# Optimization experiments

Measured on AMD Instinct MI355X. Metric: run time of the kernel, lower is better.

## Reference

```python
import jax, jax.numpy as jnp
import numpy as np

EMB = 1024
NEG_INF = float(-2**32 + 1)
EPS_SCALE = 1e-8   # epsilon added to sqrt(scale) in attention_dot
LN_EPS = 1e-5      # torch.nn.LayerNorm default eps


def _layernorm(x, w, b):
    mu = jnp.mean(x, axis=-1, keepdims=True)
    var = jnp.mean(jnp.square(x - mu), axis=-1, keepdims=True)
    return (x - mu) * jax.lax.rsqrt(var + LN_EPS) * w + b


def setup_inputs() -> dict:
    key = jax.random.key(0)
    ks = jax.random.split(key, 6)
    B, Lq, Lk, E = 8, 2048, 2048, EMB
    queries = jax.random.normal(ks[0], (B, Lq, E), dtype=jnp.float32)
    keys = jax.random.normal(ks[1], (B, Lk, E), dtype=jnp.float32)
    query_masks = jnp.ones((B, Lq), dtype=jnp.float32)
    key_masks = jnp.ones((B, Lk), dtype=jnp.float32)
    # xavier_uniform for Linear(E, E): limit = sqrt(6/(E+E))
    lim = float(np.sqrt(6.0 / (E + E)))
    W1 = jax.random.uniform(ks[2], (E, E), minval=-lim, maxval=lim, dtype=jnp.float32)
    b1 = jnp.zeros((E,), dtype=jnp.float32)
    W2 = jax.random.uniform(ks[3], (E, E), minval=-lim, maxval=lim, dtype=jnp.float32)
    b2 = jnp.zeros((E,), dtype=jnp.float32)
    ln_w = jnp.ones((E,), dtype=jnp.float32)
    ln_b = jnp.zeros((E,), dtype=jnp.float32)
    ln2_w = jnp.ones((E,), dtype=jnp.float32)
    ln2_b = jnp.zeros((E,), dtype=jnp.float32)
    return {"queries": queries, "keys": keys, "query_masks": query_masks,
            "key_masks": key_masks, "ln_w": ln_w, "ln_b": ln_b,
            "ln2_w": ln2_w, "ln2_b": ln2_b, "W1": W1, "b1": b1,
            "W2": W2, "b2": b2}


def reference(queries, keys, query_masks, key_masks, ln_w, ln_b, ln2_w, ln2_b, W1, b1, W2, b2):
    E = queries.shape[-1]
    # scores [B, Lq, Lk]
    sim = jnp.einsum('bik,bjk->bij', queries, keys)
    sim = sim / (jnp.sqrt(jnp.float32(max(1.0, E))) + EPS_SCALE)
    # key mask applied pre-softmax
    sim = jnp.where(key_masks[:, None, :] == 0, jnp.float32(NEG_INF), sim)
    sim = jax.nn.softmax(sim, axis=-1)
    # query mask applied post-softmax
    sim = sim * query_masks[:, :, None]
    attn_out = jnp.einsum('bij,bjk->bik', sim, keys)
    # residual + LayerNorm
    x = _layernorm(attn_out + queries, ln_w, ln_b)
    # FFN: Linear -> ReLU -> Linear, residual, LayerNorm
    h = jax.nn.relu(x @ W1.T + b1)
    y = h @ W2.T + b2
    return _layernorm(y + x, ln2_w, ln2_b)
```

## Files before the change

kernel.cpp:

```cpp
#include <hip/hip_runtime.h>
#include <hip/hip_bf16.h>
#include <stdint.h>

#define NB    8
#define LQ    2048
#define LKK   2048
#define EMBD  1024

typedef __bf16 bf16_t;
typedef __bf16 bf16x8 __attribute__((ext_vector_type(8)));
typedef __bf16 bf16x4 __attribute__((ext_vector_type(4)));
typedef float  f32x4  __attribute__((ext_vector_type(4)));

__device__ __forceinline__ bf16_t f2bf(float x) {
  union { float f; uint32_t u; } v; v.f = x;
  uint32_t r = v.u + 0x7fffu + ((v.u >> 16) & 1u);
  uint16_t h = (uint16_t)(r >> 16);
  return __builtin_bit_cast(bf16_t, h);
}

__device__ __forceinline__ float wred_sum(float v) {
#pragma unroll
  for (int o = 32; o; o >>= 1) v += __shfl_xor(v, o);
  return v;
}
__device__ __forceinline__ float wred_max(float v) {
#pragma unroll
  for (int o = 32; o; o >>= 1) v = fmaxf(v, __shfl_xor(v, o));
  return v;
}

template<int EPI>
__global__ __launch_bounds__(512, 2)
void gemm_nt(const bf16_t* __restrict__ A, const bf16_t* __restrict__ B,
             float* __restrict__ Cf, bf16_t* __restrict__ Cb,
             const float* __restrict__ bias, float scale,
             int M, int N, int K, long sA, long sB, long sC)
{
  __shared__ __align__(16) bf16_t Al[2][8][256][8];
  __shared__ __align__(16) bf16_t Bl[2][8][256][8];

  const int tid  = threadIdx.x;
  const int lane = tid & 63;
  const int wave = tid >> 6;
  const int bz   = blockIdx.z;

  const bf16_t* Ab = A + (long)bz * sA;
  const bf16_t* Bb = B + (long)bz * sB;

  const int bm = blockIdx.x * 256;
  const int bn = blockIdx.y * 256;
  const int wm = (wave >> 2) * 128;
  const int wn = (wave & 3) * 64;

  f32x4 acc[8][4] = {};

  const int srow = tid & 255;
  const int sslc = tid >> 8;

  const int fr = lane & 15;
  const int fs = lane >> 4;

  auto STAGE = [&](int bufi, int kt) {
#pragma unroll
    for (int i = 0; i < 4; i++) {
      const int slc = sslc + 2 * i;
      __builtin_amdgcn_global_load_lds(
        (const __attribute__((address_space(1))) void*)(Ab + (long)(bm + srow) * K + kt + slc * 8),
        (__attribute__((address_space(3))) void*)((char*)&Al[bufi][0][0][0] + (tid + i * 512) * 16),
        16, 0, 0);
    }
#pragma unroll
    for (int i = 0; i < 4; i++) {
      const int slc = sslc + 2 * i;
      __builtin_amdgcn_global_load_lds(
        (const __attribute__((address_space(1))) void*)(Bb + (long)(bn + srow) * K + kt + slc * 8),
        (__attribute__((address_space(3))) void*)((char*)&Bl[bufi][0][0][0] + (tid + i * 512) * 16),
        16, 0, 0);
    }
  };

  auto COMPUTE = [&](int bufi) {
#pragma unroll
    for (int kk = 0; kk < 2; kk++) {
      bf16x8 af[8], bfg[4];
#pragma unroll
      for (int m = 0; m < 8; m++)
        af[m] = *(const bf16x8*)&Al[bufi][4 * kk + fs][wm + m * 16 + fr][0];
#pragma unroll
      for (int n = 0; n < 4; n++)
        bfg[n] = *(const bf16x8*)&Bl[bufi][4 * kk + fs][wn + n * 16 + fr][0];
#pragma unroll
      for (int m = 0; m < 8; m++)
#pragma unroll
        for (int n = 0; n < 4; n++)
          acc[m][n] = __builtin_amdgcn_mfma_f32_16x16x32_bf16(af[m], bfg[n], acc[m][n], 0, 0, 0);
    }
  };

  STAGE(0, 0);
  __syncthreads();
  int buf = 0;
  for (int kt = 64; kt < K; kt += 64) {
    STAGE(buf ^ 1, kt);
    COMPUTE(buf);
    __syncthreads();
    buf ^= 1;
  }
  COMPUTE(buf);

  const int r0 = bm + wm + ((lane >> 4) << 2);
  const int c0 = bn + wn + fr;
  const long cb = (long)bz * sC;
#pragma unroll
  for (int n = 0; n < 4; n++) {
    const int col = c0 + n * 16;
    float bv = 0.0f;
    if constexpr (EPI >= 2) bv = bias[col];
#pragma unroll
    for (int m = 0; m < 8; m++) {
#pragma unroll
      for (int j = 0; j < 4; j++) {
        const int row = r0 + m * 16 + j;
        const long idx = cb + (long)row * N + col;
        float v = acc[m][n][j];
        if constexpr (EPI == 0)      { Cb[idx] = f2bf(v * scale); }
        else if constexpr (EPI == 1) { Cb[idx] = f2bf(v); }
        else if constexpr (EPI == 2) { v += bv; Cb[idx] = f2bf(fmaxf(v, 0.0f)); }
        else                         { v += bv; Cf[idx] = v; }
      }
    }
  }
}

__global__ __launch_bounds__(256)
void softmax_kernel(const bf16_t* __restrict__ S, bf16_t* __restrict__ P,
                    const float* __restrict__ km, const float* __restrict__ qm)
{
  __shared__ float red[8];
  const int r = blockIdx.x;
  const int b = r >> 11;
  const int t = threadIdx.x;
  const bf16_t* row = S + (long)r * LKK;

  const bf16x8 sv = *(const bf16x8*)(row + t * 8);
  const float4 k0 = ((const float4*)(km + (long)b * LKK))[2 * t];
  const float4 k1 = ((const float4*)(km + (long)b * LKK))[2 * t + 1];
  const float kmv[8] = {k0.x, k0.y, k0.z, k0.w, k1.x, k1.y, k1.z, k1.w};

  float v[8];
  float mx = -3.4e38f;
#pragma unroll
  for (int i = 0; i < 8; i++) {
    float s = (float)sv[i];
    s = (kmv[i] == 0.0f) ? -4294967295.0f : s;
    v[i] = s;
    mx = fmaxf(mx, s);
  }
  mx = wred_max(mx);
  if ((t & 63) == 0) red[t >> 6] = mx;
  __syncthreads();
  mx = fmaxf(fmaxf(red[0], red[1]), fmaxf(red[2], red[3]));

  float sum = 0.0f;
#pragma unroll
  for (int i = 0; i < 8; i++) {
    const float e = __expf(v[i] - mx);
    v[i] = e;
    sum += e;
  }
  sum = wred_sum(sum);
  if ((t & 63) == 0) red[4 + (t >> 6)] = sum;
  __syncthreads();
  sum = red[4] + red[5] + red[6] + red[7];

  const float rs = qm[r] / sum;
  bf16x8 o;
#pragma unroll
  for (int i = 0; i < 8; i++) o[i] = f2bf(v[i] * rs);
  *(bf16x8*)(P + (long)r * LKK + t * 8) = o;
}

template<int MODE>
__global__ __launch_bounds__(256)
void ln_kernel(const void* __restrict__ Xv, const void* __restrict__ Rv,
               const float* __restrict__ w, const float* __restrict__ bp,
               void* __restrict__ Yv)
{
  __shared__ float red[8];
  const long r = blockIdx.x;
  const int t = threadIdx.x;

  float x0, x1, x2, x3;
  if constexpr (MODE & 1) {
    const bf16x4 xv = ((const bf16x4*)((const bf16_t*)Xv + r * EMBD))[t];
    x0 = (float)xv[0]; x1 = (float)xv[1]; x2 = (float)xv[2]; x3 = (float)xv[3];
  } else {
    const float4 xv = ((const float4*)((const float*)Xv + r * EMBD))[t];
    x0 = xv.x; x1 = xv.y; x2 = xv.z; x3 = xv.w;
  }
  float r0, r1, r2, r3;
  if constexpr (MODE & 2) {
    const bf16x4 rv = ((const bf16x4*)((const bf16_t*)Rv + r * EMBD))[t];
    r0 = (float)rv[0]; r1 = (float)rv[1]; r2 = (float)rv[2]; r3 = (float)rv[3];
  } else {
    const float4 rv = ((const float4*)((const float*)Rv + r * EMBD))[t];
    r0 = rv.x; r1 = rv.y; r2 = rv.z; r3 = rv.w;
  }
  const float s0 = x0 + r0, s1 = x1 + r1, s2 = x2 + r2, s3 = x3 + r3;

  float sum = wred_sum(s0 + s1 + s2 + s3);
  if ((t & 63) == 0) red[t >> 6] = sum;
  __syncthreads();
  const float mu = (red[0] + red[1] + red[2] + red[3]) * (1.0f / EMBD);

  const float d0 = s0 - mu, d1 = s1 - mu, d2 = s2 - mu, d3 = s3 - mu;
  float sq = wred_sum(d0 * d0 + d1 * d1 + d2 * d2 + d3 * d3);
  if ((t & 63) == 0) red[4 + (t >> 6)] = sq;
  __syncthreads();
  const float var = (red[4] + red[5] + red[6] + red[7]) * (1.0f / EMBD);
  const float rstd = rsqrtf(var + 1e-5f);

  const float4 wv = ((const float4*)w)[t];
  const float4 bv = ((const float4*)bp)[t];
  const float y0 = d0 * rstd * wv.x + bv.x;
  const float y1 = d1 * rstd * wv.y + bv.y;
  const float y2 = d2 * rstd * wv.z + bv.z;
  const float y3 = d3 * rstd * wv.w + bv.w;

  if constexpr (MODE & 4) {
    bf16x4 o; o[0] = f2bf(y0); o[1] = f2bf(y1); o[2] = f2bf(y2); o[3] = f2bf(y3);
    ((bf16x4*)((bf16_t*)Yv + r * EMBD))[t] = o;
  } else {
    ((float4*)((float*)Yv + r * EMBD))[t] = make_float4(y0, y1, y2, y3);
  }
}

__global__ void cvt_kernel(const float* __restrict__ in, bf16_t* __restrict__ out, long n4)
{
  long i = (long)blockIdx.x * 256 + threadIdx.x;
  const long stride = (long)gridDim.x * 256;
  for (; i < n4; i += stride) {
    const float4 v = ((const float4*)in)[i];
    bf16x4 o; o[0] = f2bf(v.x); o[1] = f2bf(v.y); o[2] = f2bf(v.z); o[3] = f2bf(v.w);
    ((bf16x4*)out)[i] = o;
  }
}

__global__ __launch_bounds__(256)
void transpose_cvt(const float* __restrict__ in, bf16_t* __restrict__ out,
                   int rows, int cols)
{
  __shared__ bf16_t tile[32][33];
  const long zb = (long)blockIdx.z * rows * cols;
  const int cb = blockIdx.x * 32;
  const int rb = blockIdx.y * 32;
  const int tx = threadIdx.x & 31;
  const int ty = threadIdx.x >> 5;
#pragma unroll
  for (int i = 0; i < 4; i++) {
    const int rr = ty + i * 8;
    tile[rr][tx] = f2bf(in[zb + (long)(rb + rr) * cols + cb + tx]);
  }
  __syncthreads();
#pragma unroll
  for (int i = 0; i < 4; i++) {
    const int cc = ty + i * 8;
    out[zb + (long)(cb + cc) * rows + rb + tx] = tile[tx][cc];
  }
}

extern "C" void kernel_launch(void* const* d_in, const int* in_sizes, int n_in,
                              void* d_out, int out_size, void* d_ws, size_t ws_size,
                              hipStream_t stream)
{
  const float* q    = (const float*)d_in[0];
  const float* k    = (const float*)d_in[1];
  const float* qm   = (const float*)d_in[2];
  const float* km   = (const float*)d_in[3];
  const float* lnw  = (const float*)d_in[4];
  const float* lnb  = (const float*)d_in[5];
  const float* ln2w = (const float*)d_in[6];
  const float* ln2b = (const float*)d_in[7];
  const float* W1   = (const float*)d_in[8];
  const float* b1   = (const float*)d_in[9];
  const float* W2   = (const float*)d_in[10];
  const float* b2   = (const float*)d_in[11];

  char* ws = (char*)d_ws;
  char* ob = (char*)d_out;
  const float scale = 0.03125f;
  const long MB = 1L << 20;
  const long QE = (long)LQ * EMBD;
  const long SS = (long)LQ * LKK;

  if (ws_size >= 100 * MB) {
    bf16_t* Qb   = (bf16_t*)ws;
    bf16_t* attn = (bf16_t*)ws;
    bf16_t* Kb   = (bf16_t*)(ws + 32 * MB);
    bf16_t* h    = (bf16_t*)(ws + 32 * MB);
    bf16_t* Kt   = (bf16_t*)(ws + 64 * MB);
    bf16_t* W1b  = (bf16_t*)(ws + 96 * MB);
    bf16_t* W2b  = (bf16_t*)(ws + 98 * MB);
    bf16_t* Sb   = (bf16_t*)ob;
    float*  y    = (float*)ob;

    cvt_kernel<<<1024, 256, 0, stream>>>(W1, W1b, (long)EMBD * EMBD / 4);
    cvt_kernel<<<1024, 256, 0, stream>>>(W2, W2b, (long)EMBD * EMBD / 4);
    cvt_kernel<<<4096, 256, 0, stream>>>(q, Qb, (long)NB * QE / 4);
    cvt_kernel<<<4096, 256, 0, stream>>>(k, Kb, (long)NB * QE / 4);
    transpose_cvt<<<dim3(EMBD / 32, LKK / 32, NB), 256, 0, stream>>>(k, Kt, LKK, EMBD);

    gemm_nt<0><<<dim3(LQ / 256, LKK / 256, NB), 512, 0, stream>>>(
        Qb, Kb, nullptr, Sb, nullptr, scale, LQ, LKK, EMBD, QE, QE, SS);
    softmax_kernel<<<NB * LQ, 256, 0, stream>>>(Sb, Sb, km, qm);
    gemm_nt<1><<<dim3(LQ / 256, EMBD / 256, NB), 512, 0, stream>>>(
        Sb, Kt, nullptr, attn, nullptr, 0.0f, LQ, EMBD, LKK, SS, (long)EMBD * LKK, QE);
    ln_kernel<5><<<NB * LQ, 256, 0, stream>>>(attn, q, lnw, lnb, attn);
    gemm_nt<2><<<dim3(NB * LQ / 256, EMBD / 256, 1), 512, 0, stream>>>(
        attn, W1b, nullptr, h, b1, 0.0f, NB * LQ, EMBD, EMBD, 0, 0, 0);
    gemm_nt<3><<<dim3(NB * LQ / 256, EMBD / 256, 1), 512, 0, stream>>>(
        h, W2b, y, nullptr, b2, 0.0f, NB * LQ, EMBD, EMBD, 0, 0, 0);
    ln_kernel<2><<<NB * LQ, 256, 0, stream>>>(y, attn, ln2w, ln2b, y);

  } else if (ws_size >= 52 * MB) {
    bf16_t* attn = (bf16_t*)ws;
    bf16_t* W1b  = (bf16_t*)(ws + 32 * MB);
    bf16_t* W2b  = (bf16_t*)(ws + 34 * MB);
    bf16_t* Kth  = (bf16_t*)(ws + 36 * MB);
    bf16_t* h    = (bf16_t*)(ws + 36 * MB);
    bf16_t* Sb   = (bf16_t*)ob;
    bf16_t* Qbh  = (bf16_t*)(ob + 32 * MB);
    bf16_t* Kbh  = (bf16_t*)(ob + 48 * MB);
    float*  y    = (float*)ob;

    cvt_kernel<<<1024, 256, 0, stream>>>(W1, W1b, (long)EMBD * EMBD / 4);
    cvt_kernel<<<1024, 256, 0, stream>>>(W2, W2b, (long)EMBD * EMBD / 4);

    for (int it = 0; it < 2; it++) {
      const int bo = it * 4;
      const float* qh = q + bo * QE;
      const float* kh = k + bo * QE;
      cvt_kernel<<<2048, 256, 0, stream>>>(qh, Qbh, 4 * QE / 4);
      cvt_kernel<<<2048, 256, 0, stream>>>(kh, Kbh, 4 * QE / 4);
      transpose_cvt<<<dim3(EMBD / 32, LKK / 32, 4), 256, 0, stream>>>(kh, Kth, LKK, EMBD);

      gemm_nt<0><<<dim3(LQ / 256, LKK / 256, 4), 512, 0, stream>>>(
          Qbh, Kbh, nullptr, Sb, nullptr, scale, LQ, LKK, EMBD, QE, QE, SS);
      softmax_kernel<<<4 * LQ, 256, 0, stream>>>(Sb, Sb, km + bo * LKK, qm + bo * LQ);
      gemm_nt<1><<<dim3(LQ / 256, EMBD / 256, 4), 512, 0, stream>>>(
          Sb, Kth, nullptr, attn + bo * QE, nullptr, 0.0f, LQ, EMBD, LKK,
          SS, (long)EMBD * LKK, QE);
    }
    ln_kernel<5><<<NB * LQ, 256, 0, stream>>>(attn, q, lnw, lnb, attn);
    for (int c = 0; c < 2; c++) {
      bf16_t* xc = attn + (long)c * 8192 * EMBD;
      float*  yc = y + (long)c * 8192 * EMBD;
      gemm_nt<2><<<dim3(8192 / 256, EMBD / 256, 1), 512, 0, stream>>>(
          xc, W1b, nullptr, h, b1, 0.0f, 8192, EMBD, EMBD, 0, 0, 0);
      gemm_nt<3><<<dim3(8192 / 256, EMBD / 256, 1), 512, 0, stream>>>(
          h, W2b, yc, nullptr, b2, 0.0f, 8192, EMBD, EMBD, 0, 0, 0);
    }
    ln_kernel<2><<<NB * LQ, 256, 0, stream>>>(y, attn, ln2w, ln2b, y);

  } else {
    if (ws_size < 44 * MB) return;
    bf16_t* attn = (bf16_t*)ws;
    bf16_t* W1b  = (bf16_t*)(ws + 32 * MB);
    bf16_t* W2b  = (bf16_t*)(ws + 34 * MB);
    bf16_t* h    = (bf16_t*)(ws + 36 * MB);
    bf16_t* Sb   = (bf16_t*)(ob);
    bf16_t* Pb   = (bf16_t*)(ob + 8 * MB);
    bf16_t* Qbb  = (bf16_t*)(ob + 16 * MB);
    bf16_t* Kbb  = (bf16_t*)(ob + 20 * MB);
    bf16_t* Ktb  = (bf16_t*)(ob + 24 * MB);

    cvt_kernel<<<1024, 256, 0, stream>>>(W1, W1b, (long)EMBD * EMBD / 4);
    cvt_kernel<<<1024, 256, 0, stream>>>(W2, W2b, (long)EMBD * EMBD / 4);

    for (int b = 0; b < NB; b++) {
      const float* qb = q + b * QE;
      const float* kb = k + b * QE;
      cvt_kernel<<<2048, 256, 0, stream>>>(qb, Qbb, QE / 4);
      cvt_kernel<<<2048, 256, 0, stream>>>(kb, Kbb, QE / 4);
      transpose_cvt<<<dim3(EMBD / 32, LKK / 32, 1), 256, 0, stream>>>(kb, Ktb, LKK, EMBD);

      gemm_nt<0><<<dim3(LQ / 256, LKK / 256, 1), 512, 0, stream>>>(
          Qbb, Kbb, nullptr, Sb, nullptr, scale, LQ, LKK, EMBD, 0, 0, 0);
      softmax_kernel<<<LQ, 256, 0, stream>>>(Sb, Pb, km + (long)b * LKK, qm + (long)b * LQ);
      gemm_nt<1><<<dim3(LQ / 256, EMBD / 256, 1), 512, 0, stream>>>(
          Pb, Ktb, nullptr, attn + b * QE, nullptr, 0.0f, LQ, EMBD, LKK, 0, 0, 0);
    }
    ln_kernel<5><<<NB * LQ, 256, 0, stream>>>(attn, q, lnw, lnb, attn);
    for (int c = 0; c < 4; c++) {
      bf16_t* xc = attn + (long)c * 4096 * EMBD;
      float*  yc = (float*)d_out + (long)c * 4096 * EMBD;
      gemm_nt<2><<<dim3(4096 / 256, EMBD / 256, 1), 512, 0, stream>>>(
          xc, W1b, nullptr, h, b1, 0.0f, 4096, EMBD, EMBD, 0, 0, 0);
      gemm_nt<3><<<dim3(4096 / 256, EMBD / 256, 1), 512, 0, stream>>>(
          h, W2b, yc, nullptr, b2, 0.0f, 4096, EMBD, EMBD, 0, 0, 0);
      ln_kernel<2><<<4096, 256, 0, stream>>>(yc, xc, ln2w, ln2b, yc);
    }
  }
}
```

Before: 518.6 us.

## Deepen GEMM pipeline to four LDS stages with XCD-aware block remap

Replaces the two-buffer, K=64 staging loop with a four-buffer ring of K=32 tiles, keeping three tiles of async global-to-LDS loads in flight. Explicit vmcnt waits and one barrier per step replace the wait-all barrier. The flat block index is also remapped so consecutive tiles go to the same XCD for better L2 reuse, and MFMA issue priority is raised during compute. The cost is more barriers per K and a hand-tuned wait count that must match the number of loads issued per stage.

```diff
diff --git a/kernel.cpp b/kernel.cpp
--- a/kernel.cpp
+++ b/kernel.cpp
@@ -37,19 +37,26 @@
              const float* __restrict__ bias, float scale,
              int M, int N, int K, long sA, long sB, long sC)
 {
-  __shared__ __align__(16) bf16_t Al[2][8][256][8];
-  __shared__ __align__(16) bf16_t Bl[2][8][256][8];
+  __shared__ __align__(16) bf16_t Al[4][4][256][8];
+  __shared__ __align__(16) bf16_t Bl[4][4][256][8];
 
   const int tid  = threadIdx.x;
   const int lane = tid & 63;
   const int wave = tid >> 6;
-  const int bz   = blockIdx.z;
+
+  const int nbx = gridDim.x, nby = gridDim.y;
+  const int total = nbx * nby * gridDim.z;
+  int f = ((int)blockIdx.z * nby + (int)blockIdx.y) * nbx + (int)blockIdx.x;
+  if ((total & 7) == 0) { const int cpx = total >> 3; f = (f & 7) * cpx + (f >> 3); }
+  const int bxi = f % nbx;
+  const int byi = (f / nbx) % nby;
+  const int bz  = f / (nbx * nby);
 
   const bf16_t* Ab = A + (long)bz * sA;
   const bf16_t* Bb = B + (long)bz * sB;
 
-  const int bm = blockIdx.x * 256;
-  const int bn = blockIdx.y * 256;
+  const int bm = bxi * 256;
+  const int bn = byi * 256;
   const int wm = (wave >> 2) * 128;
   const int wn = (wave & 3) * 64;
 
@@ -62,52 +69,53 @@
   const int fs = lane >> 4;
 
   auto STAGE = [&](int bufi, int kt) {
-#pragma unroll
-    for (int i = 0; i < 4; i++) {
+    char* abase = (char*)&Al[bufi][0][0][0];
+    char* bbase = (char*)&Bl[bufi][0][0][0];
+#pragma unroll
+    for (int i = 0; i < 2; i++) {
       const int slc = sslc + 2 * i;
       __builtin_amdgcn_global_load_lds(
         (const __attribute__((address_space(1))) void*)(Ab + (long)(bm + srow) * K + kt + slc * 8),
-        (__attribute__((address_space(3))) void*)((char*)&Al[bufi][0][0][0] + (tid + i * 512) * 16),
+        (__attribute__((address_space(3))) void*)(abase + (tid + i * 512) * 16),
         16, 0, 0);
-    }
-#pragma unroll
-    for (int i = 0; i < 4; i++) {
-      const int slc = sslc + 2 * i;
       __builtin_amdgcn_global_load_lds(
         (const __attribute__((address_space(1))) void*)(Bb + (long)(bn + srow) * K + kt + slc * 8),
-        (__attribute__((address_space(3))) void*)((char*)&Bl[bufi][0][0][0] + (tid + i * 512) * 16),
+        (__attribute__((address_space(3))) void*)(bbase + (tid + i * 512) * 16),
         16, 0, 0);
     }
   };
 
   auto COMPUTE = [&](int bufi) {
-#pragma unroll
-    for (int kk = 0; kk < 2; kk++) {
-      bf16x8 af[8], bfg[4];
-#pragma unroll
-      for (int m = 0; m < 8; m++)
-        af[m] = *(const bf16x8*)&Al[bufi][4 * kk + fs][wm + m * 16 + fr][0];
+    bf16x8 af[8], bfg[4];
+#pragma unroll
+    for (int m = 0; m < 8; m++)
+      af[m] = *(const bf16x8*)&Al[bufi][fs][wm + m * 16 + fr][0];
+#pragma unroll
+    for (int n = 0; n < 4; n++)
+      bfg[n] = *(const bf16x8*)&Bl[bufi][fs][wn + n * 16 + fr][0];
+    __builtin_amdgcn_s_setprio(1);
+#pragma unroll
+    for (int m = 0; m < 8; m++)
 #pragma unroll
       for (int n = 0; n < 4; n++)
-        bfg[n] = *(const bf16x8*)&Bl[bufi][4 * kk + fs][wn + n * 16 + fr][0];
-#pragma unroll
-      for (int m = 0; m < 8; m++)
-#pragma unroll
-        for (int n = 0; n < 4; n++)
-          acc[m][n] = __builtin_amdgcn_mfma_f32_16x16x32_bf16(af[m], bfg[n], acc[m][n], 0, 0, 0);
-    }
+        acc[m][n] = __builtin_amdgcn_mfma_f32_16x16x32_bf16(af[m], bfg[n], acc[m][n], 0, 0, 0);
+    __builtin_amdgcn_s_setprio(0);
   };
 
-  STAGE(0, 0);
-  __syncthreads();
-  int buf = 0;
-  for (int kt = 64; kt < K; kt += 64) {
-    STAGE(buf ^ 1, kt);
-    COMPUTE(buf);
-    __syncthreads();
-    buf ^= 1;
-  }
-  COMPUTE(buf);
+  const int nt = K >> 5;
+  STAGE(0, 0); STAGE(1, 32); STAGE(2, 64);
+
+  for (int t = 0; t < nt; ++t) {
+    const int rem = nt - 1 - t;
+    __builtin_amdgcn_sched_barrier(0);
+    if (rem >= 2)      asm volatile("s_waitcnt vmcnt(8) lgkmcnt(0)" ::: "memory");
+    else if (rem == 1) asm volatile("s_waitcnt vmcnt(4) lgkmcnt(0)" ::: "memory");
+    else               asm volatile("s_waitcnt vmcnt(0) lgkmcnt(0)" ::: "memory");
+    __builtin_amdgcn_s_barrier();
+    __builtin_amdgcn_sched_barrier(0);
+    if (t + 3 < nt) STAGE((t + 3) & 3, (t + 3) << 5);
+    COMPUTE(t & 3);
+  }
 
   const int r0 = bm + wm + ((lane >> 4) << 2);
   const int c0 = bn + wn + fr;
```

Measured after the change: 617.2 us. 19.0% more time.

## Add smaller-tile GEMM for PV and FFN, XCD block swizzle, fuse K conversions

Applied to the files above, without the earlier changes.

Adds a 128x128-tile GEMM variant with 256 threads and three blocks per CU, used for the P·V and both FFN GEMMs. Those GEMMs have N=1024 and produce few 256x256 tiles, so the smaller tiles are meant to improve occupancy and CU balance. Both GEMM kernels now remap the flat block index so consecutive tiles land on the same XCD, which is meant to improve L2 reuse. The transpose kernel also writes the non-transposed bf16 K copy, removing a separate conversion pass over K. The trade-off is less data reuse per tile and more tile loads from global memory.

```diff
diff --git a/kernel.cpp b/kernel.cpp
--- a/kernel.cpp
+++ b/kernel.cpp
@@ -28,6 +28,11 @@
 #pragma unroll
   for (int o = 32; o; o >>= 1) v = fmaxf(v, __shfl_xor(v, o));
   return v;
+}
+
+__device__ __forceinline__ int xcd_swizzle(int f, int total) {
+  if ((total & 7) == 0) { const int cpx = total >> 3; f = (f & 7) * cpx + (f >> 3); }
+  return f;
 }
 
 template<int EPI>
@@ -43,13 +48,19 @@
   const int tid  = threadIdx.x;
   const int lane = tid & 63;
   const int wave = tid >> 6;
-  const int bz   = blockIdx.z;
+
+  const int nbx = gridDim.x, nby = gridDim.y;
+  const int f = xcd_swizzle(((int)blockIdx.z * nby + (int)blockIdx.y) * nbx + (int)blockIdx.x,
+                            nbx * nby * gridDim.z);
+  const int bxi = f % nbx;
+  const int byi = (f / nbx) % nby;
+  const int bz  = f / (nbx * nby);
 
   const bf16_t* Ab = A + (long)bz * sA;
   const bf16_t* Bb = B + (long)bz * sB;
 
-  const int bm = blockIdx.x * 256;
-  const int bn = blockIdx.y * 256;
+  const int bm = bxi * 256;
+  const int bn = byi * 256;
   const int wm = (wave >> 2) * 128;
   const int wn = (wave & 3) * 64;
 
@@ -133,6 +144,108 @@
   }
 }
 
+template<int EPI>
+__global__ __launch_bounds__(256, 3)
+void gemm_sm(const bf16_t* __restrict__ A, const bf16_t* __restrict__ B,
+             float* __restrict__ Cf, bf16_t* __restrict__ Cb,
+             const float* __restrict__ bias, float scale,
+             int M, int N, int K, long sA, long sB, long sC)
+{
+  __shared__ __align__(16) bf16_t Al[2][4][128][8];
+  __shared__ __align__(16) bf16_t Bl[2][4][128][8];
+
+  const int tid  = threadIdx.x;
+  const int lane = tid & 63;
+  const int wave = tid >> 6;
+
+  const int nbx = gridDim.x, nby = gridDim.y;
+  const int f = xcd_swizzle(((int)blockIdx.z * nby + (int)blockIdx.y) * nbx + (int)blockIdx.x,
+                            nbx * nby * gridDim.z);
+  const int bxi = f % nbx;
+  const int byi = (f / nbx) % nby;
+  const int bz  = f / (nbx * nby);
+
+  const bf16_t* Ab = A + (long)bz * sA;
+  const bf16_t* Bb = B + (long)bz * sB;
+
+  const int bm = bxi * 128;
+  const int bn = byi * 128;
+  const int wm = (wave >> 1) * 64;
+  const int wn = (wave & 1) * 64;
+
+  f32x4 acc[4][4] = {};
+
+  const int srow = tid & 127;
+  const int sslc = tid >> 7;
+
+  const int fr = lane & 15;
+  const int fs = lane >> 4;
+
+  auto STAGE = [&](int bufi, int kt) {
+#pragma unroll
+    for (int i = 0; i < 2; i++) {
+      const int slc = sslc + 2 * i;
+      __builtin_amdgcn_global_load_lds(
+        (const __attribute__((address_space(1))) void*)(Ab + (long)(bm + srow) * K + kt + slc * 8),
+        (__attribute__((address_space(3))) void*)((char*)&Al[bufi][0][0][0] + (tid + i * 256) * 16),
+        16, 0, 0);
+      __builtin_amdgcn_global_load_lds(
+        (const __attribute__((address_space(1))) void*)(Bb + (long)(bn + srow) * K + kt + slc * 8),
+        (__attribute__((address_space(3))) void*)((char*)&Bl[bufi][0][0][0] + (tid + i * 256) * 16),
+        16, 0, 0);
+    }
+  };
+
+  auto COMPUTE = [&](int bufi) {
+    bf16x8 af[4], bfg[4];
+#pragma unroll
+    for (int m = 0; m < 4; m++)
+      af[m] = *(const bf16x8*)&Al[bufi][fs][wm + m * 16 + fr][0];
+#pragma unroll
+    for (int n = 0; n < 4; n++)
+      bfg[n] = *(const bf16x8*)&Bl[bufi][fs][wn + n * 16 + fr][0];
+#pragma unroll
+    for (int m = 0; m < 4; m++)
+#pragma unroll
+      for (int n = 0; n < 4; n++)
+        acc[m][n] = __builtin_amdgcn_mfma_f32_16x16x32_bf16(af[m], bfg[n], acc[m][n], 0, 0, 0);
+  };
+
+  STAGE(0, 0);
+  __syncthreads();
+  int buf = 0;
+  for (int kt = 32; kt < K; kt += 32) {
+    STAGE(buf ^ 1, kt);
+    COMPUTE(buf);
+    __syncthreads();
+    buf ^= 1;
+  }
+  COMPUTE(buf);
+
+  const int r0 = bm + wm + ((lane >> 4) << 2);
+  const int c0 = bn + wn + fr;
+  const long cb = (long)bz * sC;
+#pragma unroll
+  for (int n = 0; n < 4; n++) {
+    const int col = c0 + n * 16;
+    float bv = 0.0f;
+    if constexpr (EPI >= 2) bv = bias[col];
+#pragma unroll
+    for (int m = 0; m < 4; m++) {
+#pragma unroll
+      for (int j = 0; j < 4; j++) {
+        const int row = r0 + m * 16 + j;
+        const long idx = cb + (long)row * N + col;
+        float v = acc[m][n][j];
+        if constexpr (EPI == 0)      { Cb[idx] = f2bf(v * scale); }
+        else if constexpr (EPI == 1) { Cb[idx] = f2bf(v); }
+        else if constexpr (EPI == 2) { v += bv; Cb[idx] = f2bf(fmaxf(v, 0.0f)); }
+        else                         { v += bv; Cf[idx] = v; }
+      }
+    }
+  }
+}
+
 __global__ __launch_bounds__(256)
 void softmax_kernel(const bf16_t* __restrict__ S, bf16_t* __restrict__ P,
                     const float* __restrict__ km, const float* __restrict__ qm)
@@ -248,8 +361,8 @@
 }
 
 __global__ __launch_bounds__(256)
-void transpose_cvt(const float* __restrict__ in, bf16_t* __restrict__ out,
-                   int rows, int cols)
+void transpose_cvt(const float* __restrict__ in, bf16_t* __restrict__ outT,
+                   bf16_t* __restrict__ outS, int rows, int cols)
 {
   __shared__ bf16_t tile[32][33];
   const long zb = (long)blockIdx.z * rows * cols;
@@ -260,13 +373,15 @@
 #pragma unroll
   for (int i = 0; i < 4; i++) {
     const int rr = ty + i * 8;
-    tile[rr][tx] = f2bf(in[zb + (long)(rb + rr) * cols + cb + tx]);
+    const bf16_t v = f2bf(in[zb + (long)(rb + rr) * cols + cb + tx]);
+    tile[rr][tx] = v;
+    if (outS != nullptr) outS[zb + (long)(rb + rr) * cols + cb + tx] = v;
   }
   __syncthreads();
 #pragma unroll
   for (int i = 0; i < 4; i++) {
     const int cc = ty + i * 8;
-    out[zb + (long)(cb + cc) * rows + rb + tx] = tile[tx][cc];
+    outT[zb + (long)(cb + cc) * rows + rb + tx] = tile[tx][cc];
   }
 }
 
@@ -308,18 +423,17 @@
     cvt_kernel<<<1024, 256, 0, stream>>>(W1, W1b, (long)EMBD * EMBD / 4);
     cvt_kernel<<<1024, 256, 0, stream>>>(W2, W2b, (long)EMBD * EMBD / 4);
     cvt_kernel<<<4096, 256, 0, stream>>>(q, Qb, (long)NB * QE / 4);
-    cvt_kernel<<<4096, 256, 0, stream>>>(k, Kb, (long)NB * QE / 4);
-    transpose_cvt<<<dim3(EMBD / 32, LKK / 32, NB), 256, 0, stream>>>(k, Kt, LKK, EMBD);
+    transpose_cvt<<<dim3(EMBD / 32, LKK / 32, NB), 256, 0, stream>>>(k, Kt, Kb, LKK, EMBD);
 
     gemm_nt<0><<<dim3(LQ / 256, LKK / 256, NB), 512, 0, stream>>>(
         Qb, Kb, nullptr, Sb, nullptr, scale, LQ, LKK, EMBD, QE, QE, SS);
     softmax_kernel<<<NB * LQ, 256, 0, stream>>>(Sb, Sb, km, qm);
-    gemm_nt<1><<<dim3(LQ / 256, EMBD / 256, NB), 512, 0, stream>>>(
+    gemm_sm<1><<<dim3(LQ / 128, EMBD / 128, NB), 256, 0, stream>>>(
         Sb, Kt, nullptr, attn, nullptr, 0.0f, LQ, EMBD, LKK, SS, (long)EMBD * LKK, QE);
     ln_kernel<5><<<NB * LQ, 256, 0, stream>>>(attn, q, lnw, lnb, attn);
-    gemm_nt<2><<<dim3(NB * LQ / 256, EMBD / 256, 1), 512, 0, stream>>>(
+    gemm_sm<2><<<dim3(NB * LQ / 128, EMBD / 128, 1), 256, 0, stream>>>(
         attn, W1b, nullptr, h, b1, 0.0f, NB * LQ, EMBD, EMBD, 0, 0, 0);
-    gemm_nt<3><<<dim3(NB * LQ / 256, EMBD / 256, 1), 512, 0, stream>>>(
+    gemm_sm<3><<<dim3(NB * LQ / 128, EMBD / 128, 1), 256, 0, stream>>>(
         h, W2b, y, nullptr, b2, 0.0f, NB * LQ, EMBD, EMBD, 0, 0, 0);
     ln_kernel<2><<<NB * LQ, 256, 0, stream>>>(y, attn, ln2w, ln2b, y);
 
@@ -342,13 +456,12 @@
       const float* qh = q + bo * QE;
       const float* kh = k + bo * QE;
       cvt_kernel<<<2048, 256, 0, stream>>>(qh, Qbh, 4 * QE / 4);
-      cvt_kernel<<<2048, 256, 0, stream>>>(kh, Kbh, 4 * QE / 4);
-      transpose_cvt<<<dim3(EMBD / 32, LKK / 32, 4), 256, 0, stream>>>(kh, Kth, LKK, EMBD);
+      transpose_cvt<<<dim3(EMBD / 32, LKK / 32, 4), 256, 0, stream>>>(kh, Kth, Kbh, LKK, EMBD);
 
       gemm_nt<0><<<dim3(LQ / 256, LKK / 256, 4), 512, 0, stream>>>(
           Qbh, Kbh, nullptr, Sb, nullptr, scale, LQ, LKK, EMBD, QE, QE, SS);
       softmax_kernel<<<4 * LQ, 256, 0, stream>>>(Sb, Sb, km + bo * LKK, qm + bo * LQ);
-      gemm_nt<1><<<dim3(LQ / 256, EMBD / 256, 4), 512, 0, stream>>>(
+      gemm_sm<1><<<dim3(LQ / 128, EMBD / 128, 4), 256, 0, stream>>>(
           Sb, Kth, nullptr, attn + bo * QE, nullptr, 0.0f, LQ, EMBD, LKK,
           SS, (long)EMBD * LKK, QE);
     }
@@ -356,9 +469,9 @@
     for (int c = 0; c < 2; c++) {
       bf16_t* xc = attn + (long)c * 8192 * EMBD;
       float*  yc = y + (long)c * 8192 * EMBD;
-      gemm_nt<2><<<dim3(8192 / 256, EMBD / 256, 1), 512, 0, stream>>>(
+      gemm_sm<2><<<dim3(8192 / 128, EMBD / 128, 1), 256, 0, stream>>>(
           xc, W1b, nullptr, h, b1, 0.0f, 8192, EMBD, EMBD, 0, 0, 0);
-      gemm_nt<3><<<dim3(8192 / 256, EMBD / 256, 1), 512, 0, stream>>>(
+      gemm_sm<3><<<dim3(8192 / 128, EMBD / 128, 1), 256, 0, stream>>>(
           h, W2b, yc, nullptr, b2, 0.0f, 8192, EMBD, EMBD, 0, 0, 0);
     }
     ln_kernel<2><<<NB * LQ, 256, 0, stream>>>(y, attn, ln2w, ln2b, y);
@@ -382,22 +495,21 @@
       const float* qb = q + b * QE;
       const float* kb = k + b * QE;
       cvt_kernel<<<2048, 256, 0, stream>>>(qb, Qbb, QE / 4);
-      cvt_kernel<<<2048, 256, 0, stream>>>(kb, Kbb, QE / 4);
-      transpose_cvt<<<dim3(EMBD / 32, LKK / 32, 1), 256, 0, stream>>>(kb, Ktb, LKK, EMBD);
+      transpose_cvt<<<dim3(EMBD / 32, LKK / 32, 1), 256, 0, stream>>>(kb, Ktb, Kbb, LKK, EMBD);
 
       gemm_nt<0><<<dim3(LQ / 256, LKK / 256, 1), 512, 0, stream>>>(
           Qbb, Kbb, nullptr, Sb, nullptr, scale, LQ, LKK, EMBD, 0, 0, 0);
       softmax_kernel<<<LQ, 256, 0, stream>>>(Sb, Pb, km + (long)b * LKK, qm + (long)b * LQ);
-      gemm_nt<1><<<dim3(LQ / 256, EMBD / 256, 1), 512, 0, stream>>>(
+      gemm_sm<1><<<dim3(LQ / 128, EMBD / 128, 1), 256, 0, stream>>>(
           Pb, Ktb, nullptr, attn + b * QE, nullptr, 0.0f, LQ, EMBD, LKK, 0, 0, 0);
     }
     ln_kernel<5><<<NB * LQ, 256, 0, stream>>>(attn, q, lnw, lnb, attn);
     for (int c = 0; c < 4; c++) {
       bf16_t* xc = attn + (long)c * 4096 * EMBD;
       float*  yc = (float*)d_out + (long)c * 4096 * EMBD;
-      gemm_nt<2><<<dim3(4096 / 256, EMBD / 256, 1), 512, 0, stream>>>(
+      gemm_sm<2><<<dim3(4096 / 128, EMBD / 128, 1), 256, 0, stream>>>(
           xc, W1b, nullptr, h, b1, 0.0f, 4096, EMBD, EMBD, 0, 0, 0);
-      gemm_nt<3><<<dim3(4096 / 256, EMBD / 256, 1), 512, 0, stream>>>(
+      gemm_sm<3><<<dim3(4096 / 128, EMBD / 128, 1), 256, 0, stream>>>(
           h, W2b, yc, nullptr, b2, 0.0f, 4096, EMBD, EMBD, 0, 0, 0);
       ln_kernel<2><<<4096, 256, 0, stream>>>(yc, xc, ln2w, ln2b, yc);
     }
```

New measurement: 588.6 us. 1.13x slower.

## Stage GEMM epilogue through swizzled LDS for coalesced stores; fuse K conversions

Applied to the files above, without the earlier changes.

The GEMM epilogue now writes accumulators into a swizzled LDS slab, then reads them back as rows so each thread issues 16-byte vectorised global stores. Before, each thread wrote scattered scalar stores. The wave-to-column mapping for B fragments is interleaved so the slab layout works. LDS becomes one 128 KB buffer and launch bounds drop to one block per CU, which lowers occupancy. Separately, the transpose kernel now also writes the straight bf16 copy of K, which removes one cvt pass over K.

```diff
diff --git a/kernel.cpp b/kernel.cpp
--- a/kernel.cpp
+++ b/kernel.cpp
@@ -31,18 +31,21 @@
 }
 
 template<int EPI>
-__global__ __launch_bounds__(512, 2)
+__global__ __launch_bounds__(512, 1)
 void gemm_nt(const bf16_t* __restrict__ A, const bf16_t* __restrict__ B,
              float* __restrict__ Cf, bf16_t* __restrict__ Cb,
              const float* __restrict__ bias, float scale,
              int M, int N, int K, long sA, long sB, long sC)
 {
-  __shared__ __align__(16) bf16_t Al[2][8][256][8];
-  __shared__ __align__(16) bf16_t Bl[2][8][256][8];
+  __shared__ __align__(16) char smem[131072];
+  typedef bf16_t ldsbuf_t[8][256][8];
+  ldsbuf_t* Abuf = (ldsbuf_t*)smem;
+  ldsbuf_t* Bbuf = (ldsbuf_t*)(smem + 65536);
 
   const int tid  = threadIdx.x;
   const int lane = tid & 63;
   const int wave = tid >> 6;
+  const int wq   = wave & 3;
   const int bz   = blockIdx.z;
 
   const bf16_t* Ab = A + (long)bz * sA;
@@ -51,7 +54,6 @@
   const int bm = blockIdx.x * 256;
   const int bn = blockIdx.y * 256;
   const int wm = (wave >> 2) * 128;
-  const int wn = (wave & 3) * 64;
 
   f32x4 acc[8][4] = {};
 
@@ -67,7 +69,7 @@
       const int slc = sslc + 2 * i;
       __builtin_amdgcn_global_load_lds(
         (const __attribute__((address_space(1))) void*)(Ab + (long)(bm + srow) * K + kt + slc * 8),
-        (__attribute__((address_space(3))) void*)((char*)&Al[bufi][0][0][0] + (tid + i * 512) * 16),
+        (__attribute__((address_space(3))) void*)((char*)&Abuf[bufi][0][0][0] + (tid + i * 512) * 16),
         16, 0, 0);
     }
 #pragma unroll
@@ -75,7 +77,7 @@
       const int slc = sslc + 2 * i;
       __builtin_amdgcn_global_load_lds(
         (const __attribute__((address_space(1))) void*)(Bb + (long)(bn + srow) * K + kt + slc * 8),
-        (__attribute__((address_space(3))) void*)((char*)&Bl[bufi][0][0][0] + (tid + i * 512) * 16),
+        (__attribute__((address_space(3))) void*)((char*)&Bbuf[bufi][0][0][0] + (tid + i * 512) * 16),
         16, 0, 0);
     }
   };
@@ -86,10 +88,10 @@
       bf16x8 af[8], bfg[4];
 #pragma unroll
       for (int m = 0; m < 8; m++)
-        af[m] = *(const bf16x8*)&Al[bufi][4 * kk + fs][wm + m * 16 + fr][0];
+        af[m] = *(const bf16x8*)&Abuf[bufi][4 * kk + fs][wm + m * 16 + fr][0];
 #pragma unroll
       for (int n = 0; n < 4; n++)
-        bfg[n] = *(const bf16x8*)&Bl[bufi][4 * kk + fs][wn + n * 16 + fr][0];
+        bfg[n] = *(const bf16x8*)&Bbuf[bufi][4 * kk + fs][n * 64 + wq * 16 + fr][0];
 #pragma unroll
       for (int m = 0; m < 8; m++)
 #pragma unroll
@@ -109,25 +111,61 @@
   }
   COMPUTE(buf);
 
-  const int r0 = bm + wm + ((lane >> 4) << 2);
-  const int c0 = bn + wn + fr;
-  const long cb = (long)bz * sC;
-#pragma unroll
-  for (int n = 0; n < 4; n++) {
-    const int col = c0 + n * 16;
-    float bv = 0.0f;
-    if constexpr (EPI >= 2) bv = bias[col];
-#pragma unroll
-    for (int m = 0; m < 8; m++) {
-#pragma unroll
-      for (int j = 0; j < 4; j++) {
-        const int row = r0 + m * 16 + j;
-        const long idx = cb + (long)row * N + col;
-        float v = acc[m][n][j];
-        if constexpr (EPI == 0)      { Cb[idx] = f2bf(v * scale); }
-        else if constexpr (EPI == 1) { Cb[idx] = f2bf(v); }
-        else if constexpr (EPI == 2) { v += bv; Cb[idx] = f2bf(fmaxf(v, 0.0f)); }
-        else                         { v += bv; Cf[idx] = v; }
+  float* slab = (float*)smem;
+  const long cbase = (long)bz * sC;
+#pragma unroll
+  for (int h = 0; h < 2; h++) {
+    __syncthreads();
+#pragma unroll
+    for (int nn = 0; nn < 2; nn++) {
+      const int n = 2 * h + nn;
+      const int colb = nn * 64 + wq * 16 + fr;
+#pragma unroll
+      for (int m = 0; m < 8; m++) {
+        const int rbase = wm + m * 16 + ((lane >> 4) << 2);
+#pragma unroll
+        for (int j = 0; j < 4; j++) {
+          const int row = rbase + j;
+          slab[row * 128 + (colb ^ (((row >> 2) & 1) << 4))] = acc[m][n][j];
+        }
+      }
+    }
+    __syncthreads();
+    const int hcol = bn + h * 128;
+    if constexpr (EPI == 3) {
+#pragma unroll
+      for (int p = 0; p < 16; p++) {
+        const int row = p * 16 + (tid >> 5);
+        const int c4  = (tid & 31) * 4;
+        f32x4 v = *(const f32x4*)&slab[row * 128 + (c4 ^ (((row >> 2) & 1) << 4))];
+        const float4 bv = *(const float4*)&bias[hcol + c4];
+        v[0] += bv.x; v[1] += bv.y; v[2] += bv.z; v[3] += bv.w;
+        *(f32x4*)&Cf[cbase + (long)(bm + row) * N + hcol + c4] = v;
+      }
+    } else {
+#pragma unroll
+      for (int p = 0; p < 8; p++) {
+        const int row  = p * 32 + (tid >> 4);
+        const int c8   = (tid & 15) * 8;
+        const int flip = ((row >> 2) & 1) << 4;
+        const f32x4 v0 = *(const f32x4*)&slab[row * 128 + (c8 ^ flip)];
+        const f32x4 v1 = *(const f32x4*)&slab[row * 128 + ((c8 + 4) ^ flip)];
+        const float vv[8] = {v0[0], v0[1], v0[2], v0[3], v1[0], v1[1], v1[2], v1[3]};
+        bf16x8 o;
+        if constexpr (EPI == 0) {
+#pragma unroll
+          for (int e = 0; e < 8; e++) o[e] = f2bf(vv[e] * scale);
+        } else if constexpr (EPI == 1) {
+#pragma unroll
+          for (int e = 0; e < 8; e++) o[e] = f2bf(vv[e]);
+        } else {
+          const float4 b0 = *(const float4*)&bias[hcol + c8];
+          const float4 b1 = *(const float4*)&bias[hcol + c8 + 4];
+          const float bb[8] = {b0.x, b0.y, b0.z, b0.w, b1.x, b1.y, b1.z, b1.w};
+#pragma unroll
+          for (int e = 0; e < 8; e++) o[e] = f2bf(fmaxf(vv[e] + bb[e], 0.0f));
+        }
+        *(bf16x8*)&Cb[cbase + (long)(bm + row) * N + hcol + c8] = o;
       }
     }
   }
@@ -248,8 +286,8 @@
 }
 
 __global__ __launch_bounds__(256)
-void transpose_cvt(const float* __restrict__ in, bf16_t* __restrict__ out,
-                   int rows, int cols)
+void transpose_cvt(const float* __restrict__ in, bf16_t* __restrict__ outT,
+                   bf16_t* __restrict__ outS, int rows, int cols)
 {
   __shared__ bf16_t tile[32][33];
   const long zb = (long)blockIdx.z * rows * cols;
@@ -260,13 +298,15 @@
 #pragma unroll
   for (int i = 0; i < 4; i++) {
     const int rr = ty + i * 8;
-    tile[rr][tx] = f2bf(in[zb + (long)(rb + rr) * cols + cb + tx]);
+    const bf16_t v = f2bf(in[zb + (long)(rb + rr) * cols + cb + tx]);
+    tile[rr][tx] = v;
+    if (outS != nullptr) outS[zb + (long)(rb + rr) * cols + cb + tx] = v;
   }
   __syncthreads();
 #pragma unroll
   for (int i = 0; i < 4; i++) {
     const int cc = ty + i * 8;
-    out[zb + (long)(cb + cc) * rows + rb + tx] = tile[tx][cc];
+    outT[zb + (long)(cb + cc) * rows + rb + tx] = tile[tx][cc];
   }
 }
 
@@ -308,8 +348,7 @@
     cvt_kernel<<<1024, 256, 0, stream>>>(W1, W1b, (long)EMBD * EMBD / 4);
     cvt_kernel<<<1024, 256, 0, stream>>>(W2, W2b, (long)EMBD * EMBD / 4);
     cvt_kernel<<<4096, 256, 0, stream>>>(q, Qb, (long)NB * QE / 4);
-    cvt_kernel<<<4096, 256, 0, stream>>>(k, Kb, (long)NB * QE / 4);
-    transpose_cvt<<<dim3(EMBD / 32, LKK / 32, NB), 256, 0, stream>>>(k, Kt, LKK, EMBD);
+    transpose_cvt<<<dim3(EMBD / 32, LKK / 32, NB), 256, 0, stream>>>(k, Kt, Kb, LKK, EMBD);
 
     gemm_nt<0><<<dim3(LQ / 256, LKK / 256, NB), 512, 0, stream>>>(
         Qb, Kb, nullptr, Sb, nullptr, scale, LQ, LKK, EMBD, QE, QE, SS);
@@ -342,8 +381,7 @@
       const float* qh = q + bo * QE;
       const float* kh = k + bo * QE;
       cvt_kernel<<<2048, 256, 0, stream>>>(qh, Qbh, 4 * QE / 4);
-      cvt_kernel<<<2048, 256, 0, stream>>>(kh, Kbh, 4 * QE / 4);
-      transpose_cvt<<<dim3(EMBD / 32, LKK / 32, 4), 256, 0, stream>>>(kh, Kth, LKK, EMBD);
+      transpose_cvt<<<dim3(EMBD / 32, LKK / 32, 4), 256, 0, stream>>>(kh, Kth, Kbh, LKK, EMBD);
 
       gemm_nt<0><<<dim3(LQ / 256, LKK / 256, 4), 512, 0, stream>>>(
           Qbh, Kbh, nullptr, Sb, nullptr, scale, LQ, LKK, EMBD, QE, QE, SS);
@@ -382,8 +420,7 @@
       const float* qb = q + b * QE;
       const float* kb = k + b * QE;
       cvt_kernel<<<2048, 256, 0, stream>>>(qb, Qbb, QE / 4);
-      cvt_kernel<<<2048, 256, 0, stream>>>(kb, Kbb, QE / 4);
-      transpose_cvt<<<dim3(EMBD / 32, LKK / 32, 1), 256, 0, stream>>>(kb, Ktb, LKK, EMBD);
+      transpose_cvt<<<dim3(EMBD / 32, LKK / 32, 1), 256, 0, stream>>>(kb, Ktb, Kbb, LKK, EMBD);
 
       gemm_nt<0><<<dim3(LQ / 256, LKK / 256, 1), 512, 0, stream>>>(
           Qbb, Kbb, nullptr, Sb, nullptr, scale, LQ, LKK, EMBD, 0, 0, 0);
```

New measurement: 456.0 us. -12.1%, faster.
